# Optimization experiments

Measured on AMD Instinct MI355X. Metric: run time of the kernel, lower is better.

## Reference

```python
import jax, jax.numpy as jnp
import numpy as np

B, S, D = 16, 512, 1024
H, HD = 16, 64          # head, head_dim; attn_dim = H*HD = D
FF = 4096               # linear_dim
EPS = 1e-6              # flax LayerNorm default epsilon


def _layernorm(x, scale):
    # flax LayerNorm(use_bias=False, use_scale=True)
    m = jnp.mean(x, axis=-1, keepdims=True)
    v = jnp.mean(jnp.square(x - m), axis=-1, keepdims=True)
    return (x - m) * jax.lax.rsqrt(v + EPS) * scale


def _attention(c, wq, wk, wv, wo):
    b, s, _ = c.shape
    q = (c @ wq).reshape(b, s, H, HD)
    k = (c @ wk).reshape(b, s, H, HD)
    v = (c @ wv).reshape(b, s, H, HD)
    score = jnp.einsum('bihd,bjhd->bijh', q, k) / jnp.sqrt(jnp.asarray(HD, c.dtype))
    score = jax.nn.softmax(score, axis=2)
    out = jnp.einsum('bijh,bjhd->bihd', score, v).reshape(b, s, H * HD)
    return out @ wo


def _mlp(x, w1, b1, w2, b2):
    return jax.nn.gelu(x @ w1 + b1) @ w2 + b2


def setup_inputs() -> dict:
    key = jax.random.key(0)
    ks = jax.random.split(key, 8)
    sd = 1.0 / np.sqrt(D)
    sf = 1.0 / np.sqrt(FF)
    return {
        'x': jax.random.normal(ks[0], (B, S, D), jnp.float32),
        'wq': jax.random.normal(ks[1], (D, D), jnp.float32) * sd,
        'wk': jax.random.normal(ks[2], (D, D), jnp.float32) * sd,
        'wv': jax.random.normal(ks[3], (D, D), jnp.float32) * sd,
        'wo': jax.random.normal(ks[4], (D, D), jnp.float32) * sd,
        'ln1_scale': jnp.ones((D,), jnp.float32),
        'ln2_scale': jnp.ones((D,), jnp.float32),
        'w1': jax.random.normal(ks[5], (D, FF), jnp.float32) * sd,
        'b1': jnp.zeros((FF,), jnp.float32),
        'w2': jax.random.normal(ks[6], (FF, D), jnp.float32) * sf,
        'b2': jnp.zeros((D,), jnp.float32),
    }


def reference(x, wq, wk, wv, wo, ln1_scale, ln2_scale, w1, b1, w2, b2):
    # inference mode: dropout / stochastic depth are identity
    c = _layernorm(x, ln1_scale)
    a = _attention(c, wq, wk, wv, wo)
    x = x + a           # x + dropout(attn(c,c))
    x = x + a           # x + attn(c,c)  (source adds attention output twice)
    x = x + _mlp(_layernorm(x, ln2_scale), w1, b1, w2, b2)
    x = x + _mlp(_layernorm(x, ln2_scale), w1, b1, w2, b2)
    return x
```

## Files before the change

### kernel.cpp

```cpp
#include <hip/hip_runtime.h>
#include <hip/hip_bf16.h>

typedef _Float16 f16;
typedef _Float16 f16x8 __attribute__((ext_vector_type(8)));
typedef _Float16 f16x4 __attribute__((ext_vector_type(4)));
typedef float    f32x4 __attribute__((ext_vector_type(4)));

#define MFMA16x16x32(a, b, c) __builtin_amdgcn_mfma_f32_16x16x32_f16(a, b, c, 0, 0, 0)

typedef __attribute__((address_space(1))) const void GASV;
typedef __attribute__((address_space(3))) void LASV;

#define WAIT_LGKM0 asm volatile("s_waitcnt lgkmcnt(0)" ::: "memory")
#define WAIT_VM6   asm volatile("s_waitcnt vmcnt(6)" ::: "memory")
#define WAIT_VM8   asm volatile("s_waitcnt vmcnt(8)" ::: "memory")

__device__ inline float gelu_f(float x) {
    float z = 0.79788456080286535588f * (x + 0.044715f * x * x * x);
    float e = __expf(2.0f * z);
    float t = 1.0f - 2.0f / (e + 1.0f);
    return 0.5f * x * (1.0f + t);
}

__global__ __launch_bounds__(256) void transpose_wt(const float* __restrict__ in,
                                                    f16* __restrict__ out,
                                                    int K, int N) {
    __shared__ float tile[32][33];
    int n0 = blockIdx.x * 32, k0 = blockIdx.y * 32;
    int tx = threadIdx.x & 31, ty = threadIdx.x >> 5;
#pragma unroll
    for (int i = 0; i < 32; i += 8)
        tile[ty + i][tx] = in[(size_t)(k0 + ty + i) * N + n0 + tx];
    __syncthreads();
#pragma unroll
    for (int i = 0; i < 32; i += 8)
        out[(size_t)(n0 + ty + i) * K + k0 + tx] = (f16)tile[tx][ty + i];
}

__global__ __launch_bounds__(256) void ln_f16(const float* __restrict__ x,
                                              const float* __restrict__ g,
                                              f16* __restrict__ out) {
    int row = blockIdx.x, t = threadIdx.x;
    float4 v = ((const float4*)(x + (size_t)row * 1024))[t];
    float s  = v.x + v.y + v.z + v.w;
    float s2 = v.x * v.x + v.y * v.y + v.z * v.z + v.w * v.w;
#pragma unroll
    for (int off = 1; off < 64; off <<= 1) {
        s  += __shfl_xor(s, off);
        s2 += __shfl_xor(s2, off);
    }
    __shared__ float red[8];
    int w = t >> 6, lane = t & 63;
    if (lane == 0) { red[w] = s; red[4 + w] = s2; }
    __syncthreads();
    s  = red[0] + red[1] + red[2] + red[3];
    s2 = red[4] + red[5] + red[6] + red[7];
    float mean = s * (1.0f / 1024.0f);
    float var  = s2 * (1.0f / 1024.0f) - mean * mean;
    float r = rsqrtf(var + 1e-6f);
    float4 gv = ((const float4*)g)[t];
    f16x4 ov;
    ov[0] = (f16)((v.x - mean) * r * gv.x);
    ov[1] = (f16)((v.y - mean) * r * gv.y);
    ov[2] = (f16)((v.z - mean) * r * gv.z);
    ov[3] = (f16)((v.w - mean) * r * gv.w);
    *(f16x4*)(out + (size_t)row * 1024 + t * 4) = ov;
}

template <int BM, int EPI, int K, int N>
__global__ __launch_bounds__(512, 2) void gemm8(
    const f16* __restrict__ A, const f16* __restrict__ Bt,
    const float* __restrict__ bias, const float* __restrict__ resid,
    float* __restrict__ outF, f16* __restrict__ outH, float rscale) {
    static_assert(BM == 256 || BM == 128, "BM");
    constexpr int AH   = BM / 128;
    constexpr int MREP = BM / 32;
    constexpr int MH   = MREP / 2;
    constexpr int NT   = K / 64;

    __shared__ __align__(16) f16 lds[2][AH + 2][128 * 64];
    __shared__ __align__(16) f16 dummyb[8192];

    const int t512 = threadIdx.x;
    const int lane = t512 & 63, w = t512 >> 6;
    const int l15 = lane & 15, lg = lane >> 4;
    const int wr = w >> 2, wc = w & 3;

    const int nwg = gridDim.x;
    const int bid = blockIdx.x;
    const int swz = (bid & 7) * (nwg >> 3) + (bid >> 3);
    constexpr int nbn = N / 256;
    const int bm = swz / nbn, bn = swz % nbn;
    const int m0 = bm * BM, n0 = bn * 256;

    const int ahalf = (BM == 256) ? wr : 0;
    const int arow0 = (BM == 256) ? 0 : wr * 64;
    const int bhalf = AH + (wc >> 1);
    const int brow0 = (wc & 1) * 64;

    auto stage = [&](int kt, int half) {
        const bool dum = (kt >= NT);
        f16* dst0 = dum ? dummyb : &lds[kt & 1][half][0];
        const bool isA = (half < AH);
        const f16* Mat = isA ? A : Bt;
        const int rb = isA ? (m0 + half * 128) : (n0 + (half - AH) * 128);
#pragma unroll
        for (int u = 0; u < 2; ++u) {
            int c = u * 512 + t512;
            int cs = c ^ ((c >> 3) & 7);
            const f16* src = dum ? (A + (size_t)(c & 511) * 8)
                                 : (Mat + (size_t)(rb + (cs >> 3)) * K + kt * 64 + (cs & 7) * 8);
            __builtin_amdgcn_global_load_lds((GASV*)src, (LASV*)(dst0 + c * 8), 16, 0, 0);
        }
    };
    auto ldfrag = [&](int cur, int half, int rh, int s) -> f16x8 {
        int ps = s ^ (rh & 7);
        return *(const f16x8*)(&lds[cur][half][0] + rh * 64 + ps * 8);
    };

    f32x4 acc[MREP][4] = {};
    f16x8 faL[2][MH], faH[2][MH], fb[2][4];

#pragma unroll
    for (int h = 0; h < AH + 2; ++h) stage(0, h);
#pragma unroll
    for (int h = 0; h < AH + 2; ++h) stage(1, h);
    if (BM == 256) { WAIT_VM8; } else { WAIT_VM6; }
    __builtin_amdgcn_s_barrier();

    for (int t = 0; t < NT; ++t) {
        const int cur = t & 1;
#pragma unroll
        for (int ks = 0; ks < 2; ++ks) {
#pragma unroll
            for (int i = 0; i < MH; ++i) {
                int rh = arow0 + i * 16 + l15;
                faL[ks][i] = ldfrag(cur, ahalf, rh, ks * 4 + lg);
            }
#pragma unroll
            for (int j = 0; j < 2; ++j) {
                int rh = brow0 + j * 16 + l15;
                fb[ks][j] = ldfrag(cur, bhalf, rh, ks * 4 + lg);
            }
        }
        __builtin_amdgcn_s_barrier();
        WAIT_LGKM0;
        __builtin_amdgcn_s_setprio(1);
#pragma unroll
        for (int i = 0; i < MH; ++i)
#pragma unroll
            for (int j = 0; j < 2; ++j)
#pragma unroll
                for (int ks = 0; ks < 2; ++ks)
                    acc[i][j] = MFMA16x16x32(faL[ks][i], fb[ks][j], acc[i][j]);
        __builtin_amdgcn_s_setprio(0);
        __builtin_amdgcn_s_barrier();
#pragma unroll
        for (int ks = 0; ks < 2; ++ks)
#pragma unroll
            for (int j = 2; j < 4; ++j) {
                int rh = brow0 + j * 16 + l15;
                fb[ks][j] = ldfrag(cur, bhalf, rh, ks * 4 + lg);
            }
        __builtin_amdgcn_s_barrier();
        WAIT_LGKM0;
        __builtin_amdgcn_s_setprio(1);
#pragma unroll
        for (int i = 0; i < MH; ++i)
#pragma unroll
            for (int j = 0; j < 2; ++j)
#pragma unroll
                for (int ks = 0; ks < 2; ++ks)
                    acc[i][2 + j] = MFMA16x16x32(faL[ks][i], fb[ks][2 + j], acc[i][2 + j]);
        __builtin_amdgcn_s_setprio(0);
        __builtin_amdgcn_s_barrier();
#pragma unroll
        for (int ks = 0; ks < 2; ++ks)
#pragma unroll
            for (int i = 0; i < MH; ++i) {
                int rh = arow0 + (MH + i) * 16 + l15;
                faH[ks][i] = ldfrag(cur, ahalf, rh, ks * 4 + lg);
            }
        stage(t + 2, AH + 0);
        __builtin_amdgcn_s_barrier();
        WAIT_LGKM0;
        __builtin_amdgcn_s_setprio(1);
#pragma unroll
        for (int i = 0; i < MH; ++i)
#pragma unroll
            for (int j = 0; j < 2; ++j)
#pragma unroll
                for (int ks = 0; ks < 2; ++ks)
                    acc[MH + i][j] = MFMA16x16x32(faH[ks][i], fb[ks][j], acc[MH + i][j]);
        __builtin_amdgcn_s_setprio(0);
        __builtin_amdgcn_s_barrier();
        stage(t + 2, AH + 1);
#pragma unroll
        for (int h = 0; h < AH; ++h) stage(t + 2, h);
        __builtin_amdgcn_s_barrier();
        WAIT_LGKM0;
        __builtin_amdgcn_s_setprio(1);
#pragma unroll
        for (int i = 0; i < MH; ++i)
#pragma unroll
            for (int j = 0; j < 2; ++j)
#pragma unroll
                for (int ks = 0; ks < 2; ++ks)
                    acc[MH + i][2 + j] = MFMA16x16x32(faH[ks][i], fb[ks][2 + j], acc[MH + i][2 + j]);
        __builtin_amdgcn_s_setprio(0);
        if (BM == 256) { WAIT_VM8; } else { WAIT_VM6; }
        __builtin_amdgcn_s_barrier();
    }

#pragma unroll
    for (int mi = 0; mi < MREP; ++mi) {
#pragma unroll
        for (int ni = 0; ni < 4; ++ni) {
            int colL = n0 + wc * 64 + ni * 16 + l15;
#pragma unroll
            for (int j = 0; j < 4; ++j) {
                int rowL = m0 + ((BM == 256) ? wr * 128 : wr * 64) + mi * 16 + lg * 4 + j;
                size_t idx = (size_t)rowL * N + colL;
                float vv = acc[mi][ni][j];
                if constexpr (EPI == 0) {
                    outH[idx] = (f16)vv;
                } else if constexpr (EPI == 1) {
                    vv += bias[colL];
                    outH[idx] = (f16)gelu_f(vv);
                } else if constexpr (EPI == 2) {
                    outF[idx] = resid[idx] + rscale * vv;
                } else {
                    outF[idx] = resid[idx] + vv + bias[colL];
                }
            }
        }
    }
}

__global__ __launch_bounds__(256) void attn_f16(const f16* __restrict__ qkv,
                                                int ld, f16* __restrict__ o) {
    __shared__ __align__(16) f16 Ks[512 * 64];
    __shared__ __align__(16) f16 Vt[64 * 512];
    __shared__ __align__(16) f16 Ps[4][16 * 32];

    const int t = threadIdx.x, lane = t & 63, w = t >> 6;
    const int l15 = lane & 15, lg = lane >> 4;
    const int bh = blockIdx.x, b = bh >> 4, h = bh & 15;
    const f16* qg = qkv + (size_t)(b * 512) * ld + h * 64;
    const f16* kg = qg + 1024;
    const f16* vg = qg + 2048;

#pragma unroll
    for (int i = 0; i < 16; ++i) {
        int c = i * 256 + t, r = c >> 3, s = c & 7;
        f16x8 val = *(const f16x8*)(kg + (size_t)r * ld + s * 8);
        *(f16x8*)((char*)Ks + r * 128 + ((s ^ (r & 7)) * 16)) = val;
    }
#pragma unroll
    for (int i = 0; i < 16; ++i) {
        int c = i * 256 + t, r = c >> 3, s = c & 7;
        f16x8 val = *(const f16x8*)(vg + (size_t)r * ld + s * 8);
#pragma unroll
        for (int dd = 0; dd < 8; ++dd) {
            int d = s * 8 + dd;
            *(f16*)((char*)Vt + d * 1024 + ((r * 2) ^ ((d & 7) << 4))) = val[dd];
        }
    }
    __syncthreads();

    for (int it = 0; it < 8; ++it) {
        int q0 = it * 64 + w * 16;
        f16x8 aq[2];
#pragma unroll
        for (int kk = 0; kk < 2; ++kk)
            aq[kk] = *(const f16x8*)(qg + (size_t)(q0 + l15) * ld + kk * 32 + lg * 8);

        f32x4 sc[32] = {};
#pragma unroll
        for (int jt = 0; jt < 32; ++jt) {
#pragma unroll
            for (int kk = 0; kk < 2; ++kk) {
                int row = jt * 16 + l15;
                f16x8 bk = *(const f16x8*)((char*)Ks + row * 128 + (((kk * 4 + lg) ^ (l15 & 7)) * 16));
                sc[jt] = MFMA16x16x32(aq[kk], bk, sc[jt]);
            }
        }

        float inv_sum[4];
#pragma unroll
        for (int r4 = 0; r4 < 4; ++r4) {
            float m = sc[0][r4];
#pragma unroll
            for (int jt = 1; jt < 32; ++jt) m = fmaxf(m, sc[jt][r4]);
#pragma unroll
            for (int off = 1; off < 16; off <<= 1) m = fmaxf(m, __shfl_xor(m, off));
            float sum = 0.0f;
#pragma unroll
            for (int jt = 0; jt < 32; ++jt) {
                float p = __expf((sc[jt][r4] - m) * 0.125f);
                sc[jt][r4] = p;
                sum += p;
            }
#pragma unroll
            for (int off = 1; off < 16; off <<= 1) sum += __shfl_xor(sum, off);
            inv_sum[r4] = 1.0f / sum;
        }

        f32x4 oa[4] = {};
        f16* myPs = &Ps[w][0];
#pragma unroll
        for (int u = 0; u < 16; ++u) {
#pragma unroll
            for (int half = 0; half < 2; ++half) {
                int jt = 2 * u + half;
#pragma unroll
                for (int r4 = 0; r4 < 4; ++r4) {
                    int row = lg * 4 + r4;
                    int colb = (half * 16 + l15) * 2;
                    *(f16*)((char*)myPs + row * 64 + (colb ^ (((row >> 1) & 3) << 4))) =
                        (f16)sc[jt][r4];
                }
            }
            f16x8 pa = *(const f16x8*)((char*)myPs + l15 * 64 + ((lg ^ ((l15 >> 1) & 3)) * 16));
#pragma unroll
            for (int ct = 0; ct < 4; ++ct) {
                int vrow = ct * 16 + l15;
                f16x8 bv = *(const f16x8*)((char*)Vt + vrow * 1024 + (((u * 4 + lg) ^ (vrow & 7)) * 16));
                oa[ct] = MFMA16x16x32(pa, bv, oa[ct]);
            }
        }

#pragma unroll
        for (int ct = 0; ct < 4; ++ct)
#pragma unroll
            for (int j = 0; j < 4; ++j) {
                int row = q0 + lg * 4 + j;
                int col = h * 64 + ct * 16 + l15;
                o[(size_t)(b * 512 + row) * 1024 + col] = (f16)(oa[ct][j] * inv_sum[j]);
            }
    }
}

extern "C" void kernel_launch(void* const* d_in, const int* in_sizes, int n_in,
                              void* d_out, int out_size, void* d_ws, size_t ws_size,
                              hipStream_t stream) {
    (void)in_sizes; (void)n_in; (void)out_size; (void)ws_size;
    const float* x   = (const float*)d_in[0];
    const float* wq  = (const float*)d_in[1];
    const float* wk  = (const float*)d_in[2];
    const float* wv  = (const float*)d_in[3];
    const float* wo  = (const float*)d_in[4];
    const float* ln1 = (const float*)d_in[5];
    const float* ln2 = (const float*)d_in[6];
    const float* w1  = (const float*)d_in[7];
    const float* b1  = (const float*)d_in[8];
    const float* w2  = (const float*)d_in[9];
    const float* b2  = (const float*)d_in[10];
    float* outF = (float*)d_out;

    char* ws = (char*)d_ws;
    size_t o = 0;
    f16* WqkvT = (f16*)(ws + o); o += (size_t)3072 * 1024 * 2;
    f16* WoT   = (f16*)(ws + o); o += (size_t)1024 * 1024 * 2;
    f16* W1T   = (f16*)(ws + o); o += (size_t)4096 * 1024 * 2;
    f16* W2T   = (f16*)(ws + o); o += (size_t)1024 * 4096 * 2;
    f16* cb    = (f16*)(ws + o); o += (size_t)8192 * 1024 * 2;
    f16* qkvb  = (f16*)(ws + o); o += (size_t)8192 * 3072 * 2;
    f16* hb    = (f16*)(ws + o); o += (size_t)8192 * 4096 * 2;
    float* x2  = (float*)(ws + o); o += (size_t)8192 * 1024 * 4;

    dim3 tb(256), tg(512);
    transpose_wt<<<dim3(32, 32), tb, 0, stream>>>(wq, WqkvT, 1024, 1024);
    transpose_wt<<<dim3(32, 32), tb, 0, stream>>>(wk, WqkvT + (size_t)1024 * 1024, 1024, 1024);
    transpose_wt<<<dim3(32, 32), tb, 0, stream>>>(wv, WqkvT + (size_t)2048 * 1024, 1024, 1024);
    transpose_wt<<<dim3(32, 32), tb, 0, stream>>>(wo, WoT, 1024, 1024);
    transpose_wt<<<dim3(128, 32), tb, 0, stream>>>(w1, W1T, 1024, 4096);
    transpose_wt<<<dim3(32, 128), tb, 0, stream>>>(w2, W2T, 4096, 1024);

    ln_f16<<<8192, tb, 0, stream>>>(x, ln1, cb);
    gemm8<256, 0, 1024, 3072><<<384, tg, 0, stream>>>(cb, WqkvT, nullptr, nullptr,
                                                      nullptr, qkvb, 0.f);
    attn_f16<<<256, tb, 0, stream>>>(qkvb, 3072, cb);
    gemm8<128, 2, 1024, 1024><<<256, tg, 0, stream>>>(cb, WoT, nullptr, x,
                                                      outF, nullptr, 2.0f);
    ln_f16<<<8192, tb, 0, stream>>>(outF, ln2, cb);
    gemm8<256, 1, 1024, 4096><<<512, tg, 0, stream>>>(cb, W1T, b1, nullptr,
                                                      nullptr, hb, 0.f);
    gemm8<128, 3, 4096, 1024><<<256, tg, 0, stream>>>(hb, W2T, b2, outF,
                                                      x2, nullptr, 1.0f);
    ln_f16<<<8192, tb, 0, stream>>>(x2, ln2, cb);
    gemm8<256, 1, 1024, 4096><<<512, tg, 0, stream>>>(cb, W1T, b1, nullptr,
                                                      nullptr, hb, 0.f);
    gemm8<128, 3, 4096, 1024><<<256, tg, 0, stream>>>(hb, W2T, b2, x2,
                                                      outF, nullptr, 1.0f);
}
```

Before: 678.5 us.

## Software-pipeline GEMM LDS fragment loads into MFMA phases across tiles

Restructures the GEMM main loop so LDS fragment reads for the next quadrant, including the next k-tile's A-low and B-low fragments, are issued before the current MFMA block runs. Explicit lgkmcnt waits are dropped and sched_barriers are added so the compiler's own waits overlap LDS reads with matrix math. All next-tile global-to-LDS stages are issued together, and a vmcnt(0) wait moves to mid-iteration. This adds register pressure and makes the stronger vmcnt(0) wait a possible stall point.

Measured after the change: 632.6 us. 1.07x faster.

```diff
diff --git a/kernel.cpp b/kernel.cpp
--- a/kernel.cpp
+++ b/kernel.cpp
@@ -11,9 +11,10 @@
 typedef __attribute__((address_space(1))) const void GASV;
 typedef __attribute__((address_space(3))) void LASV;
 
-#define WAIT_LGKM0 asm volatile("s_waitcnt lgkmcnt(0)" ::: "memory")
+#define WAIT_VM0   asm volatile("s_waitcnt vmcnt(0)" ::: "memory")
 #define WAIT_VM6   asm volatile("s_waitcnt vmcnt(6)" ::: "memory")
 #define WAIT_VM8   asm volatile("s_waitcnt vmcnt(8)" ::: "memory")
+#define SB0        __builtin_amdgcn_sched_barrier(0)
 
 __device__ inline float gelu_f(float x) {
     float z = 0.79788456080286535588f * (x + 0.044715f * x * x * x);
@@ -98,117 +99,115 @@
     const int bhalf = AH + (wc >> 1);
     const int brow0 = (wc & 1) * 64;
 
-    auto stage = [&](int kt, int half) {
+    auto stage_tile = [&](int kt) {
         const bool dum = (kt >= NT);
-        f16* dst0 = dum ? dummyb : &lds[kt & 1][half][0];
-        const bool isA = (half < AH);
-        const f16* Mat = isA ? A : Bt;
-        const int rb = isA ? (m0 + half * 128) : (n0 + (half - AH) * 128);
-#pragma unroll
-        for (int u = 0; u < 2; ++u) {
-            int c = u * 512 + t512;
-            int cs = c ^ ((c >> 3) & 7);
-            const f16* src = dum ? (A + (size_t)(c & 511) * 8)
-                                 : (Mat + (size_t)(rb + (cs >> 3)) * K + kt * 64 + (cs & 7) * 8);
-            __builtin_amdgcn_global_load_lds((GASV*)src, (LASV*)(dst0 + c * 8), 16, 0, 0);
+#pragma unroll
+        for (int h = 0; h < AH + 2; ++h) {
+            f16* dst0 = dum ? dummyb : &lds[kt & 1][h][0];
+            const bool isA = (h < AH);
+            const f16* Mat = isA ? A : Bt;
+            const int rb = isA ? (m0 + h * 128) : (n0 + (h - AH) * 128);
+#pragma unroll
+            for (int u = 0; u < 2; ++u) {
+                int c = u * 512 + t512;
+                int cs = c ^ ((c >> 3) & 7);
+                const f16* src = dum ? (A + (size_t)(c & 511) * 8)
+                                     : (Mat + (size_t)(rb + (cs >> 3)) * K + kt * 64 + (cs & 7) * 8);
+                __builtin_amdgcn_global_load_lds((GASV*)src, (LASV*)(dst0 + c * 8), 16, 0, 0);
+            }
         }
     };
-    auto ldfrag = [&](int cur, int half, int rh, int s) -> f16x8 {
+    auto ldfrag = [&](int b, int half, int rh, int s) -> f16x8 {
         int ps = s ^ (rh & 7);
-        return *(const f16x8*)(&lds[cur][half][0] + rh * 64 + ps * 8);
+        return *(const f16x8*)(&lds[b][half][0] + rh * 64 + ps * 8);
     };
 
     f32x4 acc[MREP][4] = {};
     f16x8 faL[2][MH], faH[2][MH], fb[2][4];
 
-#pragma unroll
-    for (int h = 0; h < AH + 2; ++h) stage(0, h);
-#pragma unroll
-    for (int h = 0; h < AH + 2; ++h) stage(1, h);
+    stage_tile(0);
+    stage_tile(1);
     if (BM == 256) { WAIT_VM8; } else { WAIT_VM6; }
+    SB0;
     __builtin_amdgcn_s_barrier();
+#pragma unroll
+    for (int ks = 0; ks < 2; ++ks) {
+#pragma unroll
+        for (int i = 0; i < MH; ++i)
+            faL[ks][i] = ldfrag(0, ahalf, arow0 + i * 16 + l15, ks * 4 + lg);
+#pragma unroll
+        for (int j = 0; j < 2; ++j)
+            fb[ks][j] = ldfrag(0, bhalf, brow0 + j * 16 + l15, ks * 4 + lg);
+    }
 
     for (int t = 0; t < NT; ++t) {
-        const int cur = t & 1;
-#pragma unroll
-        for (int ks = 0; ks < 2; ++ks) {
-#pragma unroll
-            for (int i = 0; i < MH; ++i) {
-                int rh = arow0 + i * 16 + l15;
-                faL[ks][i] = ldfrag(cur, ahalf, rh, ks * 4 + lg);
-            }
-#pragma unroll
-            for (int j = 0; j < 2; ++j) {
-                int rh = brow0 + j * 16 + l15;
-                fb[ks][j] = ldfrag(cur, bhalf, rh, ks * 4 + lg);
-            }
-        }
-        __builtin_amdgcn_s_barrier();
-        WAIT_LGKM0;
+        const int cur = t & 1, nxt = cur ^ 1;
+#pragma unroll
+        for (int ks = 0; ks < 2; ++ks)
+#pragma unroll
+            for (int j = 2; j < 4; ++j)
+                fb[ks][j] = ldfrag(cur, bhalf, brow0 + j * 16 + l15, ks * 4 + lg);
+        SB0;
         __builtin_amdgcn_s_setprio(1);
 #pragma unroll
-        for (int i = 0; i < MH; ++i)
-#pragma unroll
-            for (int j = 0; j < 2; ++j)
-#pragma unroll
-                for (int ks = 0; ks < 2; ++ks)
+        for (int ks = 0; ks < 2; ++ks)
+#pragma unroll
+            for (int i = 0; i < MH; ++i)
+#pragma unroll
+                for (int j = 0; j < 2; ++j)
                     acc[i][j] = MFMA16x16x32(faL[ks][i], fb[ks][j], acc[i][j]);
         __builtin_amdgcn_s_setprio(0);
         __builtin_amdgcn_s_barrier();
 #pragma unroll
         for (int ks = 0; ks < 2; ++ks)
 #pragma unroll
-            for (int j = 2; j < 4; ++j) {
-                int rh = brow0 + j * 16 + l15;
-                fb[ks][j] = ldfrag(cur, bhalf, rh, ks * 4 + lg);
-            }
-        __builtin_amdgcn_s_barrier();
-        WAIT_LGKM0;
+            for (int i = 0; i < MH; ++i)
+                faH[ks][i] = ldfrag(cur, ahalf, arow0 + (MH + i) * 16 + l15, ks * 4 + lg);
+        SB0;
         __builtin_amdgcn_s_setprio(1);
 #pragma unroll
-        for (int i = 0; i < MH; ++i)
-#pragma unroll
-            for (int j = 0; j < 2; ++j)
-#pragma unroll
-                for (int ks = 0; ks < 2; ++ks)
+        for (int ks = 0; ks < 2; ++ks)
+#pragma unroll
+            for (int i = 0; i < MH; ++i)
+#pragma unroll
+                for (int j = 0; j < 2; ++j)
                     acc[i][2 + j] = MFMA16x16x32(faL[ks][i], fb[ks][2 + j], acc[i][2 + j]);
         __builtin_amdgcn_s_setprio(0);
+        WAIT_VM0;
+        SB0;
         __builtin_amdgcn_s_barrier();
 #pragma unroll
         for (int ks = 0; ks < 2; ++ks)
 #pragma unroll
-            for (int i = 0; i < MH; ++i) {
-                int rh = arow0 + (MH + i) * 16 + l15;
-                faH[ks][i] = ldfrag(cur, ahalf, rh, ks * 4 + lg);
-            }
-        stage(t + 2, AH + 0);
-        __builtin_amdgcn_s_barrier();
-        WAIT_LGKM0;
+            for (int i = 0; i < MH; ++i)
+                faL[ks][i] = ldfrag(nxt, ahalf, arow0 + i * 16 + l15, ks * 4 + lg);
+        SB0;
         __builtin_amdgcn_s_setprio(1);
 #pragma unroll
-        for (int i = 0; i < MH; ++i)
-#pragma unroll
-            for (int j = 0; j < 2; ++j)
-#pragma unroll
-                for (int ks = 0; ks < 2; ++ks)
+        for (int ks = 0; ks < 2; ++ks)
+#pragma unroll
+            for (int i = 0; i < MH; ++i)
+#pragma unroll
+                for (int j = 0; j < 2; ++j)
                     acc[MH + i][j] = MFMA16x16x32(faH[ks][i], fb[ks][j], acc[MH + i][j]);
         __builtin_amdgcn_s_setprio(0);
         __builtin_amdgcn_s_barrier();
-        stage(t + 2, AH + 1);
-#pragma unroll
-        for (int h = 0; h < AH; ++h) stage(t + 2, h);
-        __builtin_amdgcn_s_barrier();
-        WAIT_LGKM0;
+#pragma unroll
+        for (int ks = 0; ks < 2; ++ks)
+#pragma unroll
+            for (int j = 0; j < 2; ++j)
+                fb[ks][j] = ldfrag(nxt, bhalf, brow0 + j * 16 + l15, ks * 4 + lg);
+        stage_tile(t + 2);
+        SB0;
         __builtin_amdgcn_s_setprio(1);
 #pragma unroll
-        for (int i = 0; i < MH; ++i)
-#pragma unroll
-            for (int j = 0; j < 2; ++j)
-#pragma unroll
-                for (int ks = 0; ks < 2; ++ks)
+        for (int ks = 0; ks < 2; ++ks)
+#pragma unroll
+            for (int i = 0; i < MH; ++i)
+#pragma unroll
+                for (int j = 0; j < 2; ++j)
                     acc[MH + i][2 + j] = MFMA16x16x32(faH[ks][i], fb[ks][2 + j], acc[MH + i][2 + j]);
         __builtin_amdgcn_s_setprio(0);
-        if (BM == 256) { WAIT_VM8; } else { WAIT_VM6; }
         __builtin_amdgcn_s_barrier();
     }
 
```
